# Kernel optimization log

Measured on AMD Instinct MI355X. Metric: run time of the kernel, lower is better.

## Reference

```python
import jax, jax.numpy as jnp
import numpy as np

B, DIM_IN, DIM_OUT = 2048, 4096, 4096


def setup_inputs() -> dict:
    key = jax.random.key(0)
    k1, k2, k3 = jax.random.split(key, 3)
    # binary input activations (0/1), stored as int32
    x = jax.random.randint(k1, (B, DIM_IN), 0, 2, dtype=jnp.int32)
    masks = jax.random.uniform(k2, (DIM_IN, DIM_OUT)) < 0.5
    # integer thresholds in [0, dim_in)
    thresholds = jax.random.randint(k3, (DIM_OUT,), 0, DIM_IN, dtype=jnp.int32)
    return {"x": x, "masks": masks, "thresholds": thresholds}


def reference(x, masks, thresholds):
    # Original: expand x to (B, dim_in, dim_out), XNOR with masks, sum over dim_in,
    # compare vs thresholds. XNOR(a,b) = a*b + (1-a)*(1-b), so the sum over dim_in
    # is two GEMMs -- never materialize the (B, dim_in, dim_out) tensor.
    xf = x.astype(jnp.float32)              # (B, dim_in), values in {0,1}
    mf = masks.astype(jnp.float32)          # (dim_in, dim_out)
    sums = xf @ mf + (1.0 - xf) @ (1.0 - mf)  # (B, dim_out), popcount of agreements
    return sums > thresholds.astype(jnp.float32)[None, :]  # (B, dim_out) bool
```

## Files before the change

### kernel.cpp

```cpp
#include <hip/hip_runtime.h>
#include <stdint.h>

#define BB    2048
#define DIN   4096
#define DOUT  4096


using v4i  = __attribute__((ext_vector_type(4)))  int;
using v16i = __attribute__((ext_vector_type(16))) int;

__device__ __forceinline__ void async_load16(const void* g, void* l) {
    __builtin_amdgcn_global_load_lds(
        (const __attribute__((address_space(1))) unsigned int*)g,
        (__attribute__((address_space(3))) unsigned int*)l,
        16, 0, 0);
}

__device__ __forceinline__ unsigned int to_pm1(unsigned int c) {
    return c + ((c ^ 0x01010101u) * 255u);
}

__global__ void pack_all(const int* __restrict__ x,
                         const void* __restrict__ mraw,
                         char* __restrict__ x8,
                         char* __restrict__ m8T) {
    const int tid = threadIdx.x;
    if (blockIdx.x < BB) {
        const int row = blockIdx.x;
        const int4* src = (const int4*)(x + (size_t)row * DIN);
        unsigned int* dst = (unsigned int*)(x8 + (size_t)row * DIN);
        #pragma unroll
        for (int q = 0; q < 4; ++q) {
            int4 v = src[q * 256 + tid];
            unsigned int t = (unsigned int)(v.x & 1) |
                             ((unsigned int)(v.y & 1) << 8) |
                             ((unsigned int)(v.z & 1) << 16) |
                             ((unsigned int)(v.w & 1) << 24);
            dst[q * 256 + tid] = to_pm1(t);
        }
    } else {
        const int bw = blockIdx.x - BB;
        const int n0 = (bw >> 4) * 64;
        const int k0 = (bw & 15) * 256;

        __shared__ unsigned int tl[64][68];

        const unsigned char* mb = (const unsigned char*)mraw;
        const unsigned int pv = *(const unsigned int*)(mb + (tid & 63) * 4);
        const bool isU8 = __any(pv > 1u);

        const int kq4  = tid >> 2;
        const int nq16 = (tid & 3) * 16;
        unsigned int b[4][4];
        if (isU8) {
            #pragma unroll
            for (int r = 0; r < 4; ++r) {
                uint4 v = *(const uint4*)(mb + (size_t)(k0 + kq4 * 4 + r) * DOUT
                                          + n0 + nq16);
                b[r][0] = v.x; b[r][1] = v.y; b[r][2] = v.z; b[r][3] = v.w;
            }
        } else {
            const int4* m32 = (const int4*)mraw;
            #pragma unroll
            for (int r = 0; r < 4; ++r)
                #pragma unroll
                for (int q = 0; q < 4; ++q) {
                    int4 v = m32[((size_t)(k0 + kq4 * 4 + r) * DOUT
                                  + n0 + nq16 + q * 4) >> 2];
                    b[r][q] = (unsigned int)(v.x & 1) |
                              ((unsigned int)(v.y & 1) << 8) |
                              ((unsigned int)(v.z & 1) << 16) |
                              ((unsigned int)(v.w & 1) << 24);
                }
        }
        #pragma unroll
        for (int w = 0; w < 4; ++w) {
            unsigned int a0 = b[0][w], a1 = b[1][w], a2 = b[2][w], a3 = b[3][w];
            unsigned int x0 = __builtin_amdgcn_perm(a1, a0, 0x05010400u);
            unsigned int x1 = __builtin_amdgcn_perm(a3, a2, 0x05010400u);
            unsigned int x2 = __builtin_amdgcn_perm(a1, a0, 0x07030602u);
            unsigned int x3 = __builtin_amdgcn_perm(a3, a2, 0x07030602u);
            unsigned int c0 = __builtin_amdgcn_perm(x1, x0, 0x05040100u);
            unsigned int c1 = __builtin_amdgcn_perm(x1, x0, 0x07060302u);
            unsigned int c2 = __builtin_amdgcn_perm(x3, x2, 0x05040100u);
            unsigned int c3 = __builtin_amdgcn_perm(x3, x2, 0x07060302u);
            tl[nq16 + w * 4 + 0][kq4] = to_pm1(c0);
            tl[nq16 + w * 4 + 1][kq4] = to_pm1(c1);
            tl[nq16 + w * 4 + 2][kq4] = to_pm1(c2);
            tl[nq16 + w * 4 + 3][kq4] = to_pm1(c3);
        }
        __syncthreads();

        const int nr = tid >> 2;
        const int c4 = tid & 3;
        #pragma unroll
        for (int q = 0; q < 4; ++q) {
            uint4 v = *(const uint4*)&tl[nr][4 * (c4 + 4 * q)];
            *(uint4*)(m8T + (size_t)(n0 + nr) * DIN + k0 + 16 * (c4 + 4 * q)) = v;
        }
    }
}

__global__ __launch_bounds__(256)
void bgemm(const char* __restrict__ x8,
           const char* __restrict__ m8T,
           const int* __restrict__ thr,
           int* __restrict__ out) {
    const int flat = blockIdx.x;
    const int xcd  = flat & 7;
    const int idx  = flat >> 3;
    const int bm   = (xcd & 1) * 8 + (idx & 7);
    const int bn   = (xcd >> 1) * 8 + (idx >> 3);
    const int b0   = bm * 128;
    const int o0   = bn * 128;

    const int tid  = threadIdx.x;
    const int lane = tid & 63;
    const int wv   = tid >> 6;
    const int in_  = wv & 1;
    const int kh   = wv >> 1;
    const int wn   = in_ * 64;
    const int l31  = lane & 31;
    const int lh   = lane >> 5;
    const int rsw  = l31 & 7;

    __shared__ __align__(16) char lds[65536];

    auto stage = [&](int c, int buf) {
        char* bufA = lds + buf * 32768;
        char* bufB = bufA + 16384;
        const int k0 = c * 128;
        const int r8 = lane >> 3;
        const int sl = lane & 7;
        #pragma unroll
        for (int h = 0; h < 4; ++h) {
            const int r0  = wv * 32 + h * 8;
            const int row = r0 + r8;
            const int g   = sl ^ (row & 7);
            async_load16(x8 + (size_t)(b0 + row) * DIN + k0 + g * 16,
                         bufA + r0 * 128 + lane * 16);
            async_load16(m8T + (size_t)(o0 + row) * DIN + k0 + g * 16,
                         bufB + r0 * 128 + lane * 16);
        }
    };

    v16i acc[4][2];
    #pragma unroll
    for (int t = 0; t < 4; ++t)
        #pragma unroll
        for (int u = 0; u < 2; ++u)
            acc[t][u] = (v16i)(0);

    stage(0, 0);
    __syncthreads();

    for (int c = 0; c < 32; ++c) {
        const int buf = c & 1;
        if (c < 31) stage(c + 1, buf ^ 1);

        const char* bufA = lds + buf * 32768;
        const char* bufB = bufA + 16384;
        #pragma unroll
        for (int ks = 0; ks < 2; ++ks) {
            const int slot = (((kh * 4 + ks * 2 + lh) ^ rsw)) * 16;
            v4i aF[4], bF[2];
            #pragma unroll
            for (int t = 0; t < 4; ++t)
                aF[t] = *(const v4i*)&bufA[(t * 32 + l31) * 128 + slot];
            #pragma unroll
            for (int u = 0; u < 2; ++u)
                bF[u] = *(const v4i*)&bufB[(wn + u * 32 + l31) * 128 + slot];
            __builtin_amdgcn_s_setprio(1);
            #pragma unroll
            for (int t = 0; t < 4; ++t)
                #pragma unroll
                for (int u = 0; u < 2; ++u)
                    acc[t][u] = __builtin_amdgcn_mfma_i32_32x32x32_i8(
                        aF[t], bF[u], acc[t][u], 0, 0, 0);
            __builtin_amdgcn_s_setprio(0);
        }
        __syncthreads();
    }

    int* pool = (int*)lds;
    const int p = in_;
    {
        const int give0 = kh ? 0 : 2;
        const int bw_ = p * 8192 + (kh ? 0 : 1) * 4096;
        #pragma unroll
        for (int tt = 0; tt < 2; ++tt) {
            const int t = give0 + tt;
            #pragma unroll
            for (int u = 0; u < 2; ++u)
                #pragma unroll
                for (int r = 0; r < 16; ++r) {
                    const int rowl = (r & 3) + 8 * (r >> 2) + 4 * lh;
                    pool[bw_ + (tt * 32 + rowl) * 64 + u * 32 + l31] = acc[t][u][r];
                }
        }
    }
    __syncthreads();
    const int keep0 = kh ? 2 : 0;
    const int br_ = p * 8192 + kh * 4096;
    #pragma unroll
    for (int tt = 0; tt < 2; ++tt) {
        const int t = keep0 + tt;
        #pragma unroll
        for (int u = 0; u < 2; ++u)
            #pragma unroll
            for (int r = 0; r < 16; ++r) {
                const int rowl = (r & 3) + 8 * (r >> 2) + 4 * lh;
                acc[t][u][r] += pool[br_ + (tt * 32 + rowl) * 64 + u * 32 + l31];
            }
    }

    #pragma unroll
    for (int u = 0; u < 2; ++u) {
        const int o   = o0 + wn + u * 32 + l31;
        const int lim = 2 * thr[o] - DIN;
        #pragma unroll
        for (int tt = 0; tt < 2; ++tt) {
            const int t = keep0 + tt;
            #pragma unroll
            for (int r = 0; r < 16; ++r) {
                const int rowl = (r & 3) + 8 * (r >> 2) + 4 * lh;
                const int b    = b0 + kh * 64 + tt * 32 + rowl;
                out[(size_t)b * DOUT + o] = (acc[t][u][r] > lim) ? 1 : 0;
            }
        }
    }
}

extern "C" void kernel_launch(void* const* d_in, const int* in_sizes, int n_in,
                              void* d_out, int out_size, void* d_ws, size_t ws_size,
                              hipStream_t stream) {
    const int* x          = (const int*)d_in[0];
    const void* masks     = d_in[1];
    const int* thresholds = (const int*)d_in[2];
    int* out              = (int*)d_out;

    char* x8  = (char*)d_ws;
    char* m8T = (char*)d_ws + ((size_t)8 << 20);

    pack_all<<<BB + 1024, 256, 0, stream>>>(x, masks, x8, m8T);
    bgemm<<<512, 256, 0, stream>>>(x8, m8T, thresholds, out);
}
```

Measured before the change: 181.6 us.

## Use 256x128 tiles with 8 waves and triple-buffered async LDS pipeline

The GEMM block grows to 256x128 outputs with 512 threads (8 waves split 2x2 in M/N and 2-way in K), halving the grid to 256 blocks. The LDS pipeline moves from double to triple buffering with explicit vmcnt waits and a single barrier per K step, and the s_setprio hints are dropped. This aims to cut barrier stalls and raise reuse of the mask tile, at the cost of 144KB LDS per block (one block per CU) and only 256 blocks, fewer than two waves of work per CU.

```diff
diff --git a/kernel.cpp b/kernel.cpp
--- a/kernel.cpp
+++ b/kernel.cpp
@@ -101,7 +101,7 @@
     }
 }
 
-__global__ __launch_bounds__(256)
+__global__ __launch_bounds__(512)
 void bgemm(const char* __restrict__ x8,
            const char* __restrict__ m8T,
            const int* __restrict__ thr,
@@ -109,26 +109,28 @@
     const int flat = blockIdx.x;
     const int xcd  = flat & 7;
     const int idx  = flat >> 3;
-    const int bm   = (xcd & 1) * 8 + (idx & 7);
-    const int bn   = (xcd >> 1) * 8 + (idx >> 3);
-    const int b0   = bm * 128;
+    const int bm   = (xcd & 1) * 4 + (idx & 3);
+    const int bn   = (xcd >> 1) * 8 + (idx >> 2);
+    const int b0   = bm * 256;
     const int o0   = bn * 128;
 
     const int tid  = threadIdx.x;
     const int lane = tid & 63;
     const int wv   = tid >> 6;
-    const int in_  = wv & 1;
-    const int kh   = wv >> 1;
+    const int im   = wv & 1;
+    const int in_  = (wv >> 1) & 1;
+    const int kh   = wv >> 2;
+    const int wm   = im * 128;
     const int wn   = in_ * 64;
     const int l31  = lane & 31;
     const int lh   = lane >> 5;
     const int rsw  = l31 & 7;
 
-    __shared__ __align__(16) char lds[65536];
+    __shared__ __align__(16) char lds[3 * 49152];
 
     auto stage = [&](int c, int buf) {
-        char* bufA = lds + buf * 32768;
-        char* bufB = bufA + 16384;
+        char* bufA = lds + buf * 49152;
+        char* bufB = bufA + 32768;
         const int k0 = c * 128;
         const int r8 = lane >> 3;
         const int sl = lane & 7;
@@ -139,6 +141,12 @@
             const int g   = sl ^ (row & 7);
             async_load16(x8 + (size_t)(b0 + row) * DIN + k0 + g * 16,
                          bufA + r0 * 128 + lane * 16);
+        }
+        #pragma unroll
+        for (int h = 0; h < 2; ++h) {
+            const int r0  = wv * 16 + h * 8;
+            const int row = r0 + r8;
+            const int g   = sl ^ (row & 7);
             async_load16(m8T + (size_t)(o0 + row) * DIN + k0 + g * 16,
                          bufB + r0 * 128 + lane * 16);
         }
@@ -152,38 +160,38 @@
             acc[t][u] = (v16i)(0);
 
     stage(0, 0);
-    __syncthreads();
+    stage(1, 1);
 
     for (int c = 0; c < 32; ++c) {
-        const int buf = c & 1;
-        if (c < 31) stage(c + 1, buf ^ 1);
-
-        const char* bufA = lds + buf * 32768;
-        const char* bufB = bufA + 16384;
+        if (c < 31) asm volatile("s_waitcnt vmcnt(6)" ::: "memory");
+        else        asm volatile("s_waitcnt vmcnt(0)" ::: "memory");
+        __builtin_amdgcn_s_barrier();
+        if (c < 30) stage(c + 2, (c + 2) % 3);
+
+        const char* bufA = lds + (c % 3) * 49152;
+        const char* bufB = bufA + 32768;
         #pragma unroll
         for (int ks = 0; ks < 2; ++ks) {
             const int slot = (((kh * 4 + ks * 2 + lh) ^ rsw)) * 16;
             v4i aF[4], bF[2];
             #pragma unroll
             for (int t = 0; t < 4; ++t)
-                aF[t] = *(const v4i*)&bufA[(t * 32 + l31) * 128 + slot];
+                aF[t] = *(const v4i*)&bufA[(wm + t * 32 + l31) * 128 + slot];
             #pragma unroll
             for (int u = 0; u < 2; ++u)
                 bF[u] = *(const v4i*)&bufB[(wn + u * 32 + l31) * 128 + slot];
-            __builtin_amdgcn_s_setprio(1);
             #pragma unroll
             for (int t = 0; t < 4; ++t)
                 #pragma unroll
                 for (int u = 0; u < 2; ++u)
                     acc[t][u] = __builtin_amdgcn_mfma_i32_32x32x32_i8(
                         aF[t], bF[u], acc[t][u], 0, 0, 0);
-            __builtin_amdgcn_s_setprio(0);
-        }
-        __syncthreads();
-    }
+        }
+    }
+    __syncthreads();
 
     int* pool = (int*)lds;
-    const int p = in_;
+    const int p = wv & 3;
     {
         const int give0 = kh ? 0 : 2;
         const int bw_ = p * 8192 + (kh ? 0 : 1) * 4096;
@@ -224,7 +232,7 @@
             #pragma unroll
             for (int r = 0; r < 16; ++r) {
                 const int rowl = (r & 3) + 8 * (r >> 2) + 4 * lh;
-                const int b    = b0 + kh * 64 + tt * 32 + rowl;
+                const int b    = b0 + wm + kh * 64 + tt * 32 + rowl;
                 out[(size_t)b * DOUT + o] = (acc[t][u][r] > lim) ? 1 : 0;
             }
         }
@@ -243,5 +251,5 @@
     char* m8T = (char*)d_ws + ((size_t)8 << 20);
 
     pack_all<<<BB + 1024, 256, 0, stream>>>(x, masks, x8, m8T);
-    bgemm<<<512, 256, 0, stream>>>(x8, m8T, thresholds, out);
-}
+    bgemm<<<256, 512, 0, stream>>>(x8, m8T, thresholds, out);
+}
```

Result: faster. 174.0 us (-4.2%).

## Pre-swizzle operands into MFMA fragment layout and load directly to registers

Applied to the files above, without the earlier changes.

The pack kernel now writes x and masks in a fragment-major layout, so each lane's 16-byte MFMA operand for a 32-row block and 32-wide k-slice sits contiguously. The GEMM kernel drops LDS staging, barriers and the split-K LDS reduction, and loads fragments straight from global memory into registers with a two-deep register prefetch. Tiles become 256x128 per block (128x64 per wave, no k split), halving the grid to 256 blocks. In exchange, global-memory latency must be hidden by register prefetch alone, there is no cross-wave operand sharing through LDS, and the smaller grid leaves fewer blocks than CUs.

```diff
diff --git a/kernel.cpp b/kernel.cpp
--- a/kernel.cpp
+++ b/kernel.cpp
@@ -9,26 +9,20 @@
 using v4i  = __attribute__((ext_vector_type(4)))  int;
 using v16i = __attribute__((ext_vector_type(16))) int;
 
-__device__ __forceinline__ void async_load16(const void* g, void* l) {
-    __builtin_amdgcn_global_load_lds(
-        (const __attribute__((address_space(1))) unsigned int*)g,
-        (__attribute__((address_space(3))) unsigned int*)l,
-        16, 0, 0);
-}
-
 __device__ __forceinline__ unsigned int to_pm1(unsigned int c) {
     return c + ((c ^ 0x01010101u) * 255u);
 }
 
 __global__ void pack_all(const int* __restrict__ x,
                          const void* __restrict__ mraw,
-                         char* __restrict__ x8,
-                         char* __restrict__ m8T) {
+                         char* __restrict__ x8f,
+                         char* __restrict__ m8Tf) {
     const int tid = threadIdx.x;
     if (blockIdx.x < BB) {
         const int row = blockIdx.x;
+        const int rb  = row >> 5;
+        const int rl  = row & 31;
         const int4* src = (const int4*)(x + (size_t)row * DIN);
-        unsigned int* dst = (unsigned int*)(x8 + (size_t)row * DIN);
         #pragma unroll
         for (int q = 0; q < 4; ++q) {
             int4 v = src[q * 256 + tid];
@@ -36,7 +30,10 @@
                              ((unsigned int)(v.y & 1) << 8) |
                              ((unsigned int)(v.z & 1) << 16) |
                              ((unsigned int)(v.w & 1) << 24);
-            dst[q * 256 + tid] = to_pm1(t);
+            const int w   = q * 256 + tid;
+            const int off = rb * 131072 + (w >> 3) * 1024 +
+                            (rl + 32 * ((w >> 2) & 1)) * 16 + 4 * (w & 3);
+            *(unsigned int*)(x8f + off) = to_pm1(t);
         }
     } else {
         const int bw = blockIdx.x - BB;
@@ -91,58 +88,45 @@
         }
         __syncthreads();
 
-        const int nr = tid >> 2;
-        const int c4 = tid & 3;
+        const int l  = tid & 63;
+        const int wvp = tid >> 6;
         #pragma unroll
-        for (int q = 0; q < 4; ++q) {
-            uint4 v = *(const uint4*)&tl[nr][4 * (c4 + 4 * q)];
-            *(uint4*)(m8T + (size_t)(n0 + nr) * DIN + k0 + 16 * (c4 + 4 * q)) = v;
+        for (int j = 0; j < 4; ++j) {
+            const int idxc = wvp * 4 + j;
+            const int nbl  = idxc >> 3;
+            const int kpl  = idxc & 7;
+            uint4 v = *(const uint4*)&tl[nbl * 32 + (l & 31)]
+                                       [kpl * 8 + (l >> 5) * 4];
+            const size_t off = (size_t)((n0 >> 5) + nbl) * 131072 +
+                               (size_t)((k0 >> 5) + kpl) * 1024 + l * 16;
+            *(uint4*)(m8Tf + off) = v;
         }
     }
 }
 
 __global__ __launch_bounds__(256)
-void bgemm(const char* __restrict__ x8,
-           const char* __restrict__ m8T,
+void bgemm(const char* __restrict__ x8f,
+           const char* __restrict__ m8Tf,
            const int* __restrict__ thr,
            int* __restrict__ out) {
     const int flat = blockIdx.x;
     const int xcd  = flat & 7;
     const int idx  = flat >> 3;
-    const int bm   = (xcd & 1) * 8 + (idx & 7);
-    const int bn   = (xcd >> 1) * 8 + (idx >> 3);
-    const int b0   = bm * 128;
-    const int o0   = bn * 128;
+    const int bm   = (xcd & 1) * 4 + (idx & 3);
+    const int bn   = (xcd >> 1) * 8 + (idx >> 2);
 
     const int tid  = threadIdx.x;
     const int lane = tid & 63;
     const int wv   = tid >> 6;
-    const int in_  = wv & 1;
-    const int kh   = wv >> 1;
-    const int wn   = in_ * 64;
+    const int im   = wv & 1;
+    const int in_  = wv >> 1;
+    const int mrow0 = bm * 256 + im * 128;
+    const int n0w   = bn * 128 + in_ * 64;
     const int l31  = lane & 31;
     const int lh   = lane >> 5;
-    const int rsw  = l31 & 7;
 
-    __shared__ __align__(16) char lds[65536];
-
-    auto stage = [&](int c, int buf) {
-        char* bufA = lds + buf * 32768;
-        char* bufB = bufA + 16384;
-        const int k0 = c * 128;
-        const int r8 = lane >> 3;
-        const int sl = lane & 7;
-        #pragma unroll
-        for (int h = 0; h < 4; ++h) {
-            const int r0  = wv * 32 + h * 8;
-            const int row = r0 + r8;
-            const int g   = sl ^ (row & 7);
-            async_load16(x8 + (size_t)(b0 + row) * DIN + k0 + g * 16,
-                         bufA + r0 * 128 + lane * 16);
-            async_load16(m8T + (size_t)(o0 + row) * DIN + k0 + g * 16,
-                         bufB + r0 * 128 + lane * 16);
-        }
-    };
+    const char* Ab = x8f  + (size_t)(mrow0 >> 5) * 131072 + lane * 16;
+    const char* Bb = m8Tf + (size_t)(n0w  >> 5) * 131072 + lane * 16;
 
     v16i acc[4][2];
     #pragma unroll
@@ -151,80 +135,47 @@
         for (int u = 0; u < 2; ++u)
             acc[t][u] = (v16i)(0);
 
-    stage(0, 0);
-    __syncthreads();
+    v4i aC[4], bC[2], aN[4], bN[2];
 
-    for (int c = 0; c < 32; ++c) {
-        const int buf = c & 1;
-        if (c < 31) stage(c + 1, buf ^ 1);
+    #define LD(p, a, b)                                                      \
+        {                                                                    \
+            _Pragma("unroll")                                                \
+            for (int t = 0; t < 4; ++t)                                      \
+                (a)[t] = *(const v4i*)(Ab + (size_t)t * 131072 + (p) * 1024);\
+            _Pragma("unroll")                                                \
+            for (int u = 0; u < 2; ++u)                                      \
+                (b)[u] = *(const v4i*)(Bb + (size_t)u * 131072 + (p) * 1024);\
+        }
+    #define MM(a, b)                                                         \
+        {                                                                    \
+            _Pragma("unroll")                                                \
+            for (int t = 0; t < 4; ++t)                                      \
+                _Pragma("unroll")                                            \
+                for (int u = 0; u < 2; ++u)                                  \
+                    acc[t][u] = __builtin_amdgcn_mfma_i32_32x32x32_i8(       \
+                        (a)[t], (b)[u], acc[t][u], 0, 0, 0);                 \
+        }
 
-        const char* bufA = lds + buf * 32768;
-        const char* bufB = bufA + 16384;
+    LD(0, aC, bC);
+    for (int p = 0; p < 128; p += 2) {
+        LD(p + 1, aN, bN);
+        MM(aC, bC);
+        if (p + 2 < 128) LD(p + 2, aC, bC);
+        MM(aN, bN);
+    }
+    #undef LD
+    #undef MM
+
+    #pragma unroll
+    for (int u = 0; u < 2; ++u) {
+        const int o   = n0w + u * 32 + l31;
+        const int lim = 2 * thr[o] - DIN;
         #pragma unroll
-        for (int ks = 0; ks < 2; ++ks) {
-            const int slot = (((kh * 4 + ks * 2 + lh) ^ rsw)) * 16;
-            v4i aF[4], bF[2];
-            #pragma unroll
-            for (int t = 0; t < 4; ++t)
-                aF[t] = *(const v4i*)&bufA[(t * 32 + l31) * 128 + slot];
-            #pragma unroll
-            for (int u = 0; u < 2; ++u)
-                bF[u] = *(const v4i*)&bufB[(wn + u * 32 + l31) * 128 + slot];
-            __builtin_amdgcn_s_setprio(1);
-            #pragma unroll
-            for (int t = 0; t < 4; ++t)
-                #pragma unroll
-                for (int u = 0; u < 2; ++u)
-                    acc[t][u] = __builtin_amdgcn_mfma_i32_32x32x32_i8(
-                        aF[t], bF[u], acc[t][u], 0, 0, 0);
-            __builtin_amdgcn_s_setprio(0);
-        }
-        __syncthreads();
-    }
-
-    int* pool = (int*)lds;
-    const int p = in_;
-    {
-        const int give0 = kh ? 0 : 2;
-        const int bw_ = p * 8192 + (kh ? 0 : 1) * 4096;
-        #pragma unroll
-        for (int tt = 0; tt < 2; ++tt) {
-            const int t = give0 + tt;
-            #pragma unroll
-            for (int u = 0; u < 2; ++u)
-                #pragma unroll
-                for (int r = 0; r < 16; ++r) {
-                    const int rowl = (r & 3) + 8 * (r >> 2) + 4 * lh;
-                    pool[bw_ + (tt * 32 + rowl) * 64 + u * 32 + l31] = acc[t][u][r];
-                }
-        }
-    }
-    __syncthreads();
-    const int keep0 = kh ? 2 : 0;
-    const int br_ = p * 8192 + kh * 4096;
-    #pragma unroll
-    for (int tt = 0; tt < 2; ++tt) {
-        const int t = keep0 + tt;
-        #pragma unroll
-        for (int u = 0; u < 2; ++u)
+        for (int t = 0; t < 4; ++t) {
             #pragma unroll
             for (int r = 0; r < 16; ++r) {
                 const int rowl = (r & 3) + 8 * (r >> 2) + 4 * lh;
-                acc[t][u][r] += pool[br_ + (tt * 32 + rowl) * 64 + u * 32 + l31];
-            }
-    }
-
-    #pragma unroll
-    for (int u = 0; u < 2; ++u) {
-        const int o   = o0 + wn + u * 32 + l31;
-        const int lim = 2 * thr[o] - DIN;
-        #pragma unroll
-        for (int tt = 0; tt < 2; ++tt) {
-            const int t = keep0 + tt;
-            #pragma unroll
-            for (int r = 0; r < 16; ++r) {
-                const int rowl = (r & 3) + 8 * (r >> 2) + 4 * lh;
-                const int b    = b0 + kh * 64 + tt * 32 + rowl;
+                const int b    = mrow0 + t * 32 + rowl;
                 out[(size_t)b * DOUT + o] = (acc[t][u][r] > lim) ? 1 : 0;
             }
         }
@@ -239,9 +190,9 @@
     const int* thresholds = (const int*)d_in[2];
     int* out              = (int*)d_out;
 
-    char* x8  = (char*)d_ws;
-    char* m8T = (char*)d_ws + ((size_t)8 << 20);
+    char* x8f  = (char*)d_ws;
+    char* m8Tf = (char*)d_ws + ((size_t)8 << 20);
 
-    pack_all<<<BB + 1024, 256, 0, stream>>>(x, masks, x8, m8T);
-    bgemm<<<512, 256, 0, stream>>>(x8, m8T, thresholds, out);
+    pack_all<<<BB + 1024, 256, 0, stream>>>(x, masks, x8f, m8Tf);
+    bgemm<<<256, 256, 0, stream>>>(x8f, m8Tf, thresholds, out);
 }
```

Result: slower. 198.4 us (+9.2%).
